# Kernel optimization log

Measured on AMD Instinct MI355X. Metric: run time of the kernel, lower is better.

## Reference

```python
import jax, jax.numpy as jnp
import numpy as np

ANCHOR_SIZES = (128.0, 256.0, 512.0)
ANCHOR_RATIOS = (0.5, 1.0, 2.0)
IOU_THR = 0.3


def _conv(x, w, b, pad):
    y = jax.lax.conv_general_dilated(
        x, w, window_strides=(1, 1), padding=[(pad, pad), (pad, pad)],
        dimension_numbers=("NCHW", "OIHW", "NCHW"))
    return y + b[None, :, None, None]


def _make_anchors(grid_h, grid_w, stride):
    # torchvision-style cell anchors (ratio-major over scales), rounded
    scales = jnp.asarray(ANCHOR_SIZES, jnp.float32)
    ratios = jnp.asarray(ANCHOR_RATIOS, jnp.float32)
    h_r = jnp.sqrt(ratios)
    w_r = 1.0 / h_r
    ws = (w_r[:, None] * scales[None, :]).reshape(-1)  # (A,)
    hs = (h_r[:, None] * scales[None, :]).reshape(-1)
    base = jnp.round(jnp.stack([-ws, -hs, ws, hs], axis=1) / 2.0)  # (A,4)
    sx = jnp.arange(grid_w, dtype=jnp.float32) * stride
    sy = jnp.arange(grid_h, dtype=jnp.float32) * stride
    yy, xx = jnp.meshgrid(sy, sx, indexing="ij")
    shifts = jnp.stack([xx, yy, xx, yy], axis=-1).reshape(-1, 4)  # (HW,4)
    return (shifts[:, None, :] + base[None, :, :]).reshape(-1, 4)  # (HW*A,4)


def _apply_box(anchors, deltas):
    w = anchors[:, 2] - anchors[:, 0]
    h = anchors[:, 3] - anchors[:, 1]
    cx = anchors[:, 0] + 0.5 * w
    cy = anchors[:, 1] + 0.5 * h
    pcx = deltas[:, 0] * w + cx
    pcy = deltas[:, 1] * h + cy
    pw = jnp.exp(deltas[:, 2]) * w
    ph = jnp.exp(deltas[:, 3]) * h
    return jnp.stack([pcx - 0.5 * pw, pcy - 0.5 * ph,
                      pcx + 0.5 * pw, pcy + 0.5 * ph], axis=1)


def _clip(boxes, img_h, img_w):
    x1 = jnp.clip(boxes[:, 0], 0.0, img_w)
    y1 = jnp.clip(boxes[:, 1], 0.0, img_h)
    x2 = jnp.clip(boxes[:, 2], 0.0, img_w)
    y2 = jnp.clip(boxes[:, 3], 0.0, img_h)
    return jnp.stack([x1, y1, x2, y2], axis=1)


def _nms_keep(boxes, scores, thr):
    # returns boolean keep mask in ORIGINAL box order (all idxs identical in
    # the source's batched_nms call, so this is plain NMS)
    n = boxes.shape[0]
    order = jnp.argsort(-scores)
    b = boxes[order]
    area = (b[:, 2] - b[:, 0]) * (b[:, 3] - b[:, 1])
    lt = jnp.maximum(b[:, None, :2], b[None, :, :2])
    rb = jnp.minimum(b[:, None, 2:], b[None, :, 2:])
    wh = jnp.clip(rb - lt, 0.0, None)
    inter = wh[..., 0] * wh[..., 1]
    iou = inter / (area[:, None] + area[None, :] - inter + 1e-9)  # (N,N)
    idx = jnp.arange(n)

    def body(i, keep):
        sup = (iou[i] > thr) & (idx > i)
        return jnp.where(keep[i], keep & ~sup, keep)

    keep_sorted = jax.lax.fori_loop(0, n, body, jnp.ones(n, bool))
    return jnp.zeros(n, bool).at[order].set(keep_sorted)


def setup_inputs() -> dict:
    key = jax.random.key(0)
    ks = jax.random.split(key, 7)
    C, H, W = 256, 32, 32
    A = len(ANCHOR_SIZES) * len(ANCHOR_RATIOS)  # 9
    return {
        "features": jax.random.normal(ks[0], (1, C, H, W), jnp.float32),
        "image_size": 512,
        "conv_w": jax.random.normal(ks[1], (512, C, 3, 3), jnp.float32) * 0.01,
        "conv_b": jnp.zeros((512,), jnp.float32),
        "cls_w": jax.random.normal(ks[2], (2 * A, 512, 1, 1), jnp.float32) * 0.01,
        "cls_b": jnp.zeros((2 * A,), jnp.float32),
        "bbox_w": jax.random.normal(ks[3], (4 * A, 512, 1, 1), jnp.float32) * 0.01,
        "bbox_b": jnp.zeros((4 * A,), jnp.float32),
    }


def reference(features, image_size, conv_w, conv_b, cls_w, cls_b, bbox_w, bbox_b):
    img_h = img_w = float(image_size)
    x = jax.nn.relu(_conv(features, conv_w, conv_b, pad=1))
    logits = _conv(x, cls_w, cls_b, pad=0)          # (1, 2A, H, W)
    bbox_pred = _conv(x, bbox_w, bbox_b, pad=0)     # (1, 4A, H, W)
    probs = jax.nn.sigmoid(logits)
    fg_scores = probs[:, 1::2, :, :].reshape(-1)    # same flatten order as torch
    grid_h, grid_w = features.shape[2], features.shape[3]
    stride = image_size // grid_h
    anchors = _make_anchors(grid_h, grid_w, float(stride))
    proposals = _apply_box(anchors, bbox_pred.reshape(-1, 4))
    proposals = _clip(proposals, img_h, img_w)
    keep = _nms_keep(proposals, fg_scores, IOU_THR)
    # fixed-shape output: suppressed boxes zeroed, plus the keep mask
    return proposals * keep[:, None].astype(proposals.dtype), probs, keep
```

## Files before the change

### kernel.cpp

```cpp
#include <hip/hip_runtime.h>
#include <math.h>

#define X_B      0
#define BBOX_B   2097152
#define PROPS_B  2244608
#define KEYS_B   2392064
#define RANK_B   2465792
#define SKEYS_B  2502656
#define SBOX_B   2576384
#define MASK_B   2725888
#define WS_NEED  13400000

typedef unsigned long long u64;
typedef double v4d __attribute__((ext_vector_type(4)));

__global__ __launch_bounds__(256, 2) void conv3x3_mfma_k(
    const float* __restrict__ feat, const float* __restrict__ w,
    const float* __restrict__ bias, float* __restrict__ xout)
{
  __shared__ float wl[9280];
  __shared__ float fl[8768];

  const int tid = threadIdx.x;
  const int bid = blockIdx.x;
  const int ct = ((bid & 7) << 2) | ((bid >> 3) >> 4);
  const int g  = (bid >> 3) & 15;
  const int co0 = ct << 4;
  const int y0  = g << 1;

  for (int i = tid; i < 8768; i += 256) fl[i] = 0.0f;

  const int lane = tid & 63, wv = tid >> 6;
  const int q = lane >> 4, n = lane & 15;
  const int wy = wv >> 1, xb = (wv & 1) << 4;
  const int xn = xb + n;

  v4d ac0 = {0.0, 0.0, 0.0, 0.0}, ac1 = {0.0, 0.0, 0.0, 0.0};
  v4d ac2 = {0.0, 0.0, 0.0, 0.0}, ac3 = {0.0, 0.0, 0.0, 0.0};
  const float4* feat4 = (const float4*)feat;

  __syncthreads();

  for (int c = 0; c < 4; ++c) {
    const int cb = c << 6;
    #pragma unroll
    for (int i = 0; i < 9; ++i) {
      const int idx4 = tid + (i << 8);
      const int co = idx4 / 144;
      const int s4 = idx4 - co * 144;
      *(float4*)&wl[co * 580 + (s4 << 2)] =
          *(const float4*)(w + (co0 + co) * 2304 + c * 576 + (s4 << 2));
    }
    #pragma unroll
    for (int i = 0; i < 8; ++i) {
      const int idx4 = tid + (i << 8);
      const int ci = idx4 >> 5;
      const int rr = (idx4 >> 3) & 3;
      const int x4 = idx4 & 7;
      const int grow = y0 - 1 + rr;
      if ((unsigned)grow < 32u) {
        const float4 v = feat4[((cb + ci) << 8) + (grow << 3) + x4];
        float* p = &fl[ci * 137 + rr * 34 + 1 + (x4 << 2)];
        p[0] = v.x; p[1] = v.y; p[2] = v.z; p[3] = v.w;
      }
    }
    __syncthreads();
    #pragma unroll
    for (int tap = 0; tap < 9; ++tap) {
      const int ky = tap / 3, kx = tap - 3 * (tap / 3);
      const float* ab = &wl[n * 580 + q * 9 + tap];
      const float* bb = &fl[q * 137 + (wy + ky) * 34 + xn + kx];
      #pragma unroll
      for (int u = 0; u < 16; u += 4) {
        ac0 = __builtin_amdgcn_mfma_f64_16x16x4f64(
            (double)ab[(u + 0) * 36], (double)bb[(u + 0) * 548], ac0, 0, 0, 0);
        ac1 = __builtin_amdgcn_mfma_f64_16x16x4f64(
            (double)ab[(u + 1) * 36], (double)bb[(u + 1) * 548], ac1, 0, 0, 0);
        ac2 = __builtin_amdgcn_mfma_f64_16x16x4f64(
            (double)ab[(u + 2) * 36], (double)bb[(u + 2) * 548], ac2, 0, 0, 0);
        ac3 = __builtin_amdgcn_mfma_f64_16x16x4f64(
            (double)ab[(u + 3) * 36], (double)bb[(u + 3) * 548], ac3, 0, 0, 0);
      }
    }
    __syncthreads();
  }

  const int pbase = (g << 6) + (wv << 4) + n;
  #pragma unroll
  for (int i = 0; i < 4; ++i) {
    const int co = co0 + q + (i << 2);
    const double s = (ac0[i] + ac1[i]) + (ac2[i] + ac3[i]);
    const double v = fmax(s + (double)bias[co], 0.0);
    xout[(co << 10) + pbase] = (float)v;
  }
}

#define CPITCH 38
#define CCHS   (18 * CPITCH)
__global__ __launch_bounds__(256) void conv3x3_relu_fb_k(
    const float* __restrict__ feat, const float* __restrict__ w,
    const float* __restrict__ bias, float* __restrict__ xout)
{
  __shared__ float il[2][8 * CCHS];
  const int cp = blockIdx.x >> 1, h = blockIdx.x & 1;
  const int tid = threadIdx.x;
  const int h16 = h << 4;
  const int co0 = cp << 1;
  for (int i = tid; i < 8 * CCHS; i += 256) { il[0][i] = 0.0f; il[1][i] = 0.0f; }
  const int yl = tid >> 4;
  const int x0 = (tid & 15) << 1;
  double aA0 = 0.0, aA1 = 0.0, aB0 = 0.0, aB1 = 0.0;
  const float4* feat4 = (const float4*)feat;
  float4 pf[5]; int pch[5], pt[5], pc4[5], pok[5];
  #pragma unroll
  for (int k = 0; k < 5; ++k) {
    const int i = tid + (k << 8);
    const int ch = i / 144, rem = i - ch * 144;
    const int t = rem >> 3, c4 = rem & 7;
    const int g = h16 - 1 + t;
    pch[k] = ch; pt[k] = t; pc4[k] = c4;
    pok[k] = (i < 1152) && ((unsigned)g < 32u);
    pf[k] = pok[k] ? feat4[(ch << 8) + (g << 3) + c4] : float4{0.f,0.f,0.f,0.f};
  }
  __syncthreads();
  for (int cc = 0; cc < 256; cc += 8) {
    const int buf = (cc >> 3) & 1;
    #pragma unroll
    for (int k = 0; k < 5; ++k)
      if (pok[k]) {
        float* p = &il[buf][pch[k] * CCHS + pt[k] * CPITCH + (pc4[k] << 2) + 1];
        p[0] = pf[k].x; p[1] = pf[k].y; p[2] = pf[k].z; p[3] = pf[k].w;
      }
    if (cc + 8 < 256) {
      #pragma unroll
      for (int k = 0; k < 5; ++k) {
        const int g = h16 - 1 + pt[k];
        if (pok[k]) pf[k] = feat4[((cc + 8 + pch[k]) << 8) + (g << 3) + pc4[k]];
      }
    }
    __syncthreads();
    #pragma unroll
    for (int cl = 0; cl < 8; ++cl) {
      const float* wAp = w + co0 * 2304 + (cc + cl) * 9;
      const float* wBp = wAp + 2304;
      double wa[9], wb[9];
      #pragma unroll
      for (int q = 0; q < 9; ++q) { wa[q] = (double)wAp[q]; wb[q] = (double)wBp[q]; }
      const float* ir = &il[buf][cl * CCHS + yl * CPITCH + x0];
      #pragma unroll
      for (int ky = 0; ky < 3; ++ky) {
        const float2 q0 = *(const float2*)(ir + ky * CPITCH);
        const float2 q1 = *(const float2*)(ir + ky * CPITCH + 2);
        const double v0 = (double)q0.x, v1 = (double)q0.y;
        const double v2 = (double)q1.x, v3 = (double)q1.y;
        aA0 += v0 * wa[3*ky+0] + v1 * wa[3*ky+1] + v2 * wa[3*ky+2];
        aA1 += v1 * wa[3*ky+0] + v2 * wa[3*ky+1] + v3 * wa[3*ky+2];
        aB0 += v0 * wb[3*ky+0] + v1 * wb[3*ky+1] + v2 * wb[3*ky+2];
        aB1 += v1 * wb[3*ky+0] + v2 * wb[3*ky+1] + v3 * wb[3*ky+2];
      }
    }
  }
  const double bA = (double)bias[co0], bB = (double)bias[co0 + 1];
  const int y = h16 + yl;
  float2 rA, rB;
  rA.x = (float)fmax(aA0 + bA, 0.0); rA.y = (float)fmax(aA1 + bA, 0.0);
  rB.x = (float)fmax(aB0 + bB, 0.0); rB.y = (float)fmax(aB1 + bB, 0.0);
  *(float2*)&xout[(co0 << 10) + (y << 5) + x0] = rA;
  *(float2*)&xout[((co0 + 1) << 10) + (y << 5) + x0] = rB;
}

__global__ __launch_bounds__(256) void head1x1_k(
    const float* __restrict__ x,
    const float* __restrict__ cls_w, const float* __restrict__ cls_b,
    const float* __restrict__ bbox_w, const float* __restrict__ bbox_b,
    float* __restrict__ out, float* __restrict__ bbox_out)
{
  __shared__ float wl[512];
  const int bid = blockIdx.x;
  const int co = bid >> 2;
  const int px = ((bid & 3) << 8) | threadIdx.x;
  const bool is_cls = co < 18;
  const float* wsrc = is_cls ? (cls_w + co * 512) : (bbox_w + (co - 18) * 512);
  for (int i = threadIdx.x; i < 512; i += 256) wl[i] = wsrc[i];
  __syncthreads();
  double acc0 = 0.0, acc1 = 0.0, acc2 = 0.0, acc3 = 0.0;
  #pragma unroll 4
  for (int c = 0; c < 512; c += 4) {
    acc0 += (double)x[((c + 0) << 10) | px] * (double)wl[c + 0];
    acc1 += (double)x[((c + 1) << 10) | px] * (double)wl[c + 1];
    acc2 += (double)x[((c + 2) << 10) | px] * (double)wl[c + 2];
    acc3 += (double)x[((c + 3) << 10) | px] * (double)wl[c + 3];
  }
  double acc = ((acc0 + acc1) + (acc2 + acc3)) +
               (double)(is_cls ? cls_b[co] : bbox_b[co - 18]);
  if (is_cls)
    out[36864 + (co << 10) + px] = (float)(1.0 / (1.0 + exp(-acc)));
  else
    bbox_out[((co - 18) << 10) + px] = (float)acc;
}

__global__ __launch_bounds__(256) void proposals_k(
    const float* __restrict__ bbox, const int* __restrict__ imgsz,
    const float* __restrict__ out, float* __restrict__ props,
    u64* __restrict__ keys, unsigned* __restrict__ rank)
{
  const int r = blockIdx.x * 256 + threadIdx.x;
  if (r >= 9216) return;
  const float4 d = ((const float4*)bbox)[r];
  const int cell = r / 9, a = r - cell * 9;
  const int ix = cell & 31, iy = cell >> 5;
  const int ri = a / 3, si = a - ri * 3;
  const double ratio = (ri == 0) ? 0.5 : (ri == 1 ? 1.0 : 2.0);
  const double scale = (si == 0) ? 128.0 : (si == 1 ? 256.0 : 512.0);
  const double hr = sqrt(ratio), wr = 1.0 / hr;
  const double bx = nearbyint(wr * scale * 0.5);
  const double by = nearbyint(hr * scale * 0.5);
  const double cx = ix * 16.0, cy = iy * 16.0;
  const double w = 2.0 * bx, hh = 2.0 * by;
  const double pcx = (double)d.x * w + cx;
  const double pcy = (double)d.y * hh + cy;
  const double pw = exp((double)d.z) * w;
  const double ph = exp((double)d.w) * hh;
  const double im = (double)imgsz[0];
  float4 o;
  o.x = (float)fmin(fmax(pcx - 0.5 * pw, 0.0), im);
  o.y = (float)fmin(fmax(pcy - 0.5 * ph, 0.0), im);
  o.z = (float)fmin(fmax(pcx + 0.5 * pw, 0.0), im);
  o.w = (float)fmin(fmax(pcy + 0.5 * ph, 0.0), im);
  ((float4*)props)[r] = o;
  const float s = out[36864 + ((2 * (r >> 10) + 1) << 10) + (r & 1023)];
  keys[r] = ((u64)__float_as_uint(s) << 32) | (unsigned)(0x7FFFFFFF - r);
  rank[r] = 0u;
}

__global__ __launch_bounds__(256) void rank_k(
    const u64* __restrict__ keys, unsigned* __restrict__ rank)
{
  const int jt = blockIdx.x % 36, ic = blockIdx.x / 36;
  const int j = jt * 256 + threadIdx.x;
  const u64 kj = keys[j];
  const int lane = threadIdx.x & 63;
  const int base = ic * 576;
  unsigned lo[9], hi[9];
  #pragma unroll
  for (int rr = 0; rr < 9; ++rr) {
    const u64 k = keys[base + rr * 64 + lane];
    lo[rr] = (unsigned)k; hi[rr] = (unsigned)(k >> 32);
  }
  unsigned cnt = 0;
  #pragma unroll
  for (int rr = 0; rr < 9; ++rr) {
    #pragma unroll
    for (int l = 0; l < 64; ++l) {
      const unsigned llo = (unsigned)__builtin_amdgcn_readlane((int)lo[rr], l);
      const unsigned lhi = (unsigned)__builtin_amdgcn_readlane((int)hi[rr], l);
      const u64 ki = ((u64)lhi << 32) | llo;
      cnt += (ki > kj) ? 1u : 0u;
    }
  }
  atomicAdd(&rank[j], cnt);
}

__global__ __launch_bounds__(256) void scatter_k(
    const u64* __restrict__ keys, const unsigned* __restrict__ rank,
    const float* __restrict__ props, u64* __restrict__ skeys,
    float4* __restrict__ sboxes)
{
  const int r = blockIdx.x * 256 + threadIdx.x;
  if (r >= 9216) return;
  const unsigned rk = rank[r];
  skeys[rk] = keys[r];
  sboxes[rk] = ((const float4*)props)[r];
}

__global__ __launch_bounds__(256) void mask_k(
    const float4* __restrict__ sb4, u64* __restrict__ mask)
{
  __shared__ __align__(16) float4 ib[64];
  const int ci = blockIdx.x;
  const int Wb = blockIdx.y << 2;
  const int i_lo = ci << 6;
  const int i_hi = min(i_lo + 64, (Wb + 4) << 6);
  if (i_lo >= i_hi) return;
  const int wv = threadIdx.x >> 6, lane = threadIdx.x & 63;
  const int W = Wb + wv;
  const int cnt = i_hi - i_lo;
  if (threadIdx.x < cnt) ib[threadIdx.x] = sb4[i_lo + threadIdx.x];
  __syncthreads();
  const float4 bj = sb4[(W << 6) + lane];
  const float areaJ = (bj.z - bj.x) * (bj.w - bj.y);
  const int n = i_hi - i_lo;
  #pragma unroll 8
  for (int k = 0; k < n; ++k) {
    const float4 bi = ib[k];
    const float areaI = (bi.z - bi.x) * (bi.w - bi.y);
    const float ix1 = fmaxf(bj.x, bi.x), iy1 = fmaxf(bj.y, bi.y);
    const float ix2 = fminf(bj.z, bi.z), iy2 = fminf(bj.w, bi.w);
    const float iw = fmaxf(ix2 - ix1, 0.0f), ih = fmaxf(iy2 - iy1, 0.0f);
    const double inter = (double)iw * (double)ih;
    const double uni = (double)areaJ + (double)areaI - inter + 1e-9;
    const bool pred = inter > 0.3 * uni;
    const u64 bal = __ballot(pred);
    const int i = i_lo + k;
    if (lane == 0) mask[(size_t)i * 144 + W] = bal;
  }
}

__global__ __launch_bounds__(1024) void sweep_out_k(
    const u64* __restrict__ mask, const u64* __restrict__ skeys,
    const float4* __restrict__ sboxes, float* __restrict__ out)
{
  extern __shared__ __align__(16) char sm[];
  u64* subm   = (u64*)sm;
  u64* supS   = subm + 9216;
  u64* keptS  = supS + 16;
  unsigned short* kpl = (unsigned short*)(keptS + 144);
  int* kcnt  = (int*)(kpl + 9216);

  const int tid = threadIdx.x;
  const int lane = tid & 63, wv = tid >> 6;
  if (tid == 0) *kcnt = 0;
  if (tid < 144) keptS[tid] = 0ULL;
  if (tid < 16) supS[tid] = 0ULL;
  if (tid < 512) {
    const int wq = tid & 7, r0 = tid >> 3;
    #pragma unroll
    for (int k = 0; k < 8; ++k) {
      const int i = r0 + (k << 6);
      subm[i * 9 + wq] = mask[(size_t)i * 144 + wq];
    }
  }
  __syncthreads();

  int Kpp = 0, Kp = 0;

  for (int sg = 0; sg < 18; ++sg) {
    const int buf = sg & 1, nb = buf ^ 1;
    const int wbase = sg << 3;
    const int ibase = wbase << 6;
    if (wv == 0) {
      u64 dacc = 0ULL;
      {
        const int wq = lane & 7;
        int j = Kpp + (lane >> 3);
        for (; j + 24 < Kp; j += 32) {
          const u64 a0 = mask[(size_t)kpl[j +  0] * 144 + wbase + wq];
          const u64 a1 = mask[(size_t)kpl[j +  8] * 144 + wbase + wq];
          const u64 a2 = mask[(size_t)kpl[j + 16] * 144 + wbase + wq];
          const u64 a3 = mask[(size_t)kpl[j + 24] * 144 + wbase + wq];
          dacc |= (a0 | a1) | (a2 | a3);
        }
        for (; j < Kp; j += 8)
          dacc |= mask[(size_t)kpl[j] * 144 + wbase + wq];
      }
      dacc |= __shfl_xor(dacc, 8, 64);
      dacc |= __shfl_xor(dacc, 16, 64);
      dacc |= __shfl_xor(dacc, 32, 64);
      u64 myAlive = (lane < 8) ? ~(supS[(buf << 3) + lane] | dacc) : 0ULL;
      if (lane < 8) supS[(buf << 3) + lane] = 0ULL;
      const u64* sub = subm + buf * 4608;
      u64 rowL8[8];
      #pragma unroll
      for (int w = 0; w < 8; ++w)
        rowL8[w] = sub[((w << 6) + lane) * 9 + w];
      int Kcur = Kp;
      #pragma unroll
      for (int w = 0; w < 8; ++w) {
        const u64 av = __shfl(myAlive, w, 64);
        if (av == 0ULL) continue;
        const u64 rowL = rowL8[w];
        u64 cand = av, keptw = 0ULL;
        while (cand) {
          const int b = (int)__builtin_ctzll(cand);
          keptw |= 1ULL << b;
          const u64 sup =
              ((u64)(unsigned)__builtin_amdgcn_readlane((int)(rowL >> 32), b)
               << 32) |
              (unsigned)__builtin_amdgcn_readlane((int)rowL, b);
          cand &= ~(sup | (1ULL << b));
        }
        if (lane == 0) keptS[wbase + w] = keptw;
        if (keptw) {
          if ((keptw >> lane) & 1ULL) {
            const int pre =
                __builtin_popcountll(keptw & ((1ULL << lane) - 1ULL));
            kpl[Kcur + pre] = (unsigned short)(ibase + (w << 6) + lane);
          }
          Kcur += __builtin_popcountll(keptw);
          u64 t = keptw;
          while (t) {
            int bs[8]; int nn = 0;
            #pragma unroll
            for (int s = 0; s < 8; ++s) {
              if (t) { bs[s] = (int)__builtin_ctzll(t); t &= t - 1ULL; nn = s + 1; }
              else bs[s] = 0;
            }
            const int kk = lane >> 3, wq = lane & 7;
            u64 r = (kk < nn) ? sub[((w << 6) + bs[kk]) * 9 + wq] : 0ULL;
            r |= __shfl_down(r, 8, 64);
            r |= __shfl_down(r, 16, 64);
            r |= __shfl_down(r, 32, 64);
            myAlive &= ~r;
          }
        }
      }
      Kpp = Kp; Kp = Kcur;
      if (lane == 0) *kcnt = Kcur;
    } else if (wv < 12) {
      if (sg + 1 < 18) {
        const int Kh = *kcnt;
        const int t6 = tid - 64;
        const int wq = t6 & 7, str = t6 >> 3;
        const int wb2 = (sg + 1) << 3;
        u64 acc = 0ULL;
        int j = str;
        for (; j + 3 * 88 < Kh; j += 4 * 88) {
          const u64 a0 = mask[(size_t)kpl[j + 0 * 88] * 144 + wb2 + wq];
          const u64 a1 = mask[(size_t)kpl[j + 1 * 88] * 144 + wb2 + wq];
          const u64 a2 = mask[(size_t)kpl[j + 2 * 88] * 144 + wb2 + wq];
          const u64 a3 = mask[(size_t)kpl[j + 3 * 88] * 144 + wb2 + wq];
          acc |= (a0 | a1) | (a2 | a3);
        }
        for (; j < Kh; j += 88)
          acc |= mask[(size_t)kpl[j] * 144 + wb2 + wq];
        if (acc) {
          atomicOr((unsigned*)&supS[(nb << 3) + wq], (unsigned)acc);
          atomicOr(((unsigned*)&supS[(nb << 3) + wq]) + 1, (unsigned)(acc >> 32));
        }
      }
    } else if (sg + 1 < 18) {
      const int s = tid - 768;
      const int wq = s & 7, r0 = s >> 3;
      const int ib2 = (sg + 1) << 9;
      const int wb2 = (sg + 1) << 3;
      #pragma unroll
      for (int k = 0; k < 16; ++k) {
        const int i = r0 + (k << 5);
        subm[nb * 4608 + i * 9 + wq] = mask[(size_t)(ib2 + i) * 144 + wb2 + wq];
      }
    }
    __syncthreads();
  }
  for (int i = tid; i < 9216; i += 1024) {
    const u64 key = skeys[i];
    const int orig = 0x7FFFFFFF - (int)(unsigned)(key & 0xFFFFFFFFULL);
    const bool kp = (keptS[i >> 6] >> (i & 63)) & 1ULL;
    float4 ob = sboxes[i];
    if (!kp) { ob.x = 0.f; ob.y = 0.f; ob.z = 0.f; ob.w = 0.f; }
    ((float4*)out)[orig] = ob;
    out[55296 + orig] = kp ? 1.0f : 0.0f;
  }
}

__global__ __launch_bounds__(1024) void nms_fallback_k(
    const float* __restrict__ props, float* __restrict__ out)
{
  __shared__ u64 wmax[16];
  __shared__ float4 curBoxS;
  const int tid = threadIdx.x, wid = tid >> 6, lane = tid & 63;
  u64 key[9];
  float4 box[9];
  #pragma unroll
  for (int j = 0; j < 9; ++j) {
    const int r = tid + (j << 10);
    box[j] = ((const float4*)props)[r];
    const float s = out[36864 + ((2 * (r >> 10) + 1) << 10) + (r & 1023)];
    key[j] = ((u64)__float_as_uint(s) << 32) | (unsigned)(0x7FFFFFFF - r);
  }
  unsigned kept = 0;
  for (;;) {
    u64 m = key[0];
    #pragma unroll
    for (int j = 1; j < 9; ++j) m = key[j] > m ? key[j] : m;
    #pragma unroll
    for (int off = 32; off; off >>= 1) {
      const u64 o = __shfl_down(m, off, 64);
      if (o > m) m = o;
    }
    if (lane == 0) wmax[wid] = m;
    __syncthreads();
    u64 K = wmax[0];
    #pragma unroll
    for (int wv2 = 1; wv2 < 16; ++wv2) { const u64 t = wmax[wv2]; if (t > K) K = t; }
    if (K == 0) break;
    #pragma unroll
    for (int j = 0; j < 9; ++j)
      if (key[j] == K) { curBoxS = box[j]; key[j] = 0; kept |= 1u << j; }
    __syncthreads();
    const float4 cb = curBoxS;
    const float areaC = (cb.z - cb.x) * (cb.w - cb.y);
    #pragma unroll
    for (int j = 0; j < 9; ++j) {
      if (key[j]) {
        const float4 b = box[j];
        const float ix1 = fmaxf(b.x, cb.x), iy1 = fmaxf(b.y, cb.y);
        const float ix2 = fminf(b.z, cb.z), iy2 = fminf(b.w, cb.w);
        const float iw = fmaxf(ix2 - ix1, 0.0f), ih = fmaxf(iy2 - iy1, 0.0f);
        const float areaB = (b.z - b.x) * (b.w - b.y);
        const double inter = (double)iw * (double)ih;
        const double uni = (double)areaB + (double)areaC - inter + 1e-9;
        if (inter > 0.3 * uni) key[j] = 0;
      }
    }
    __syncthreads();
  }
  #pragma unroll
  for (int j = 0; j < 9; ++j) {
    const int r = tid + (j << 10);
    const bool kp = (kept >> j) & 1u;
    float4 ob = box[j];
    if (!kp) { ob.x = 0.f; ob.y = 0.f; ob.z = 0.f; ob.w = 0.f; }
    ((float4*)out)[r] = ob;
    out[55296 + r] = kp ? 1.0f : 0.0f;
  }
}

extern "C" void kernel_launch(void* const* d_in, const int* in_sizes, int n_in,
                              void* d_out, int out_size, void* d_ws, size_t ws_size,
                              hipStream_t stream)
{
  const float* feat   = (const float*)d_in[0];
  const int*   imgsz  = (const int*)d_in[1];
  const float* conv_w = (const float*)d_in[2];
  const float* conv_b = (const float*)d_in[3];
  const float* cls_w  = (const float*)d_in[4];
  const float* cls_b  = (const float*)d_in[5];
  const float* bbox_w = (const float*)d_in[6];
  const float* bbox_b = (const float*)d_in[7];
  float* out = (float*)d_out;
  char*  ws  = (char*)d_ws;
  float* x      = (float*)(ws + X_B);
  float* bbox   = (float*)(ws + BBOX_B);
  float* props  = (float*)(ws + PROPS_B);
  u64*      keys  = (u64*)(ws + KEYS_B);
  unsigned* rankp = (unsigned*)(ws + RANK_B);
  u64*      skeys = (u64*)(ws + SKEYS_B);
  float4*   sboxs = (float4*)(ws + SBOX_B);
  u64*      maskp = (u64*)(ws + MASK_B);

  if (ws_size >= (size_t)WS_NEED) {
    hipLaunchKernelGGL(conv3x3_mfma_k, dim3(512), dim3(256), 0, stream,
                       feat, conv_w, conv_b, x);
    hipLaunchKernelGGL(head1x1_k, dim3(216), dim3(256), 0, stream,
                       x, cls_w, cls_b, bbox_w, bbox_b, out, bbox);
    hipLaunchKernelGGL(proposals_k, dim3(36), dim3(256), 0, stream,
                       bbox, imgsz, out, props, keys, rankp);
    hipLaunchKernelGGL(rank_k, dim3(576), dim3(256), 0, stream, keys, rankp);
    hipLaunchKernelGGL(scatter_k, dim3(36), dim3(256), 0, stream,
                       keys, rankp, props, skeys, sboxs);
    hipLaunchKernelGGL(mask_k, dim3(144, 36), dim3(256), 0, stream,
                       sboxs, maskp);
    hipLaunchKernelGGL(sweep_out_k, dim3(1), dim3(1024), 93444, stream,
                       maskp, skeys, sboxs, out);
  } else {
    hipLaunchKernelGGL(conv3x3_relu_fb_k, dim3(512), dim3(256), 0, stream,
                       feat, conv_w, conv_b, x);
    hipLaunchKernelGGL(head1x1_k, dim3(216), dim3(256), 0, stream,
                       x, cls_w, cls_b, bbox_w, bbox_b, out, bbox);
    hipLaunchKernelGGL(proposals_k, dim3(36), dim3(256), 0, stream,
                       bbox, imgsz, out, props, keys, rankp);
    hipLaunchKernelGGL(nms_fallback_k, dim3(1), dim3(1024), 0, stream,
                       props, out);
  }
}
```

Measured before the change: 249.7 us.

## Double-buffer conv3x3 MFMA LDS tiles with register-staged prefetch

Splits the input-channel loop into eight stages of 32 channels, using two LDS buffers. Global loads for the next stage go into registers and are issued before the MFMA work on the current buffer, then written to the other buffer afterwards. This hides global-memory latency behind compute and removes one barrier per stage. The cost is extra registers for the staged float4s, which may affect occupancy under the 2-blocks launch bound.

```diff
diff --git a/kernel.cpp b/kernel.cpp
--- a/kernel.cpp
+++ b/kernel.cpp
@@ -18,8 +18,8 @@
     const float* __restrict__ feat, const float* __restrict__ w,
     const float* __restrict__ bias, float* __restrict__ xout)
 {
-  __shared__ float wl[9280];
-  __shared__ float fl[8768];
+  __shared__ float wl2[2][4672];
+  __shared__ float fl2[2][4416];
 
   const int tid = threadIdx.x;
   const int bid = blockIdx.x;
@@ -28,50 +28,74 @@
   const int co0 = ct << 4;
   const int y0  = g << 1;
 
-  for (int i = tid; i < 8768; i += 256) fl[i] = 0.0f;
-
   const int lane = tid & 63, wv = tid >> 6;
   const int q = lane >> 4, n = lane & 15;
   const int wy = wv >> 1, xb = (wv & 1) << 4;
   const int xn = xb + n;
 
+  int wco[5], ws4[5]; bool wok[5];
+  #pragma unroll
+  for (int i = 0; i < 5; ++i) {
+    const int idx4 = tid + (i << 8);
+    wok[i] = idx4 < 1152;
+    const int co = idx4 / 72;
+    wco[i] = co; ws4[i] = idx4 - co * 72;
+  }
+  int fci[4], frr[4], fx4[4]; bool fok[4];
+  #pragma unroll
+  for (int i = 0; i < 4; ++i) {
+    const int idx4 = tid + (i << 8);
+    fci[i] = idx4 >> 5; frr[i] = (idx4 >> 3) & 3; fx4[i] = idx4 & 7;
+    fok[i] = ((unsigned)(y0 - 1 + frr[i]) < 32u);
+  }
+
+  for (int i = tid; i < 2 * 4416; i += 256) ((float*)fl2)[i] = 0.0f;
+
+  const float4* feat4 = (const float4*)feat;
+  float4 wr[5], fr[4];
+
+  #pragma unroll
+  for (int i = 0; i < 5; ++i)
+    if (wok[i])
+      wr[i] = *(const float4*)(w + (co0 + wco[i]) * 2304 + (ws4[i] << 2));
+  #pragma unroll
+  for (int i = 0; i < 4; ++i)
+    if (fok[i])
+      fr[i] = feat4[(fci[i] << 8) + ((y0 - 1 + frr[i]) << 3) + fx4[i]];
+  __syncthreads();
+  #pragma unroll
+  for (int i = 0; i < 5; ++i)
+    if (wok[i]) *(float4*)&wl2[0][wco[i] * 292 + (ws4[i] << 2)] = wr[i];
+  #pragma unroll
+  for (int i = 0; i < 4; ++i)
+    if (fok[i])
+      *(float4*)&fl2[0][fci[i] * 137 + frr[i] * 34 + 1 + (fx4[i] << 2)] = fr[i];
+  __syncthreads();
+
   v4d ac0 = {0.0, 0.0, 0.0, 0.0}, ac1 = {0.0, 0.0, 0.0, 0.0};
   v4d ac2 = {0.0, 0.0, 0.0, 0.0}, ac3 = {0.0, 0.0, 0.0, 0.0};
-  const float4* feat4 = (const float4*)feat;
-
-  __syncthreads();
-
-  for (int c = 0; c < 4; ++c) {
-    const int cb = c << 6;
-    #pragma unroll
-    for (int i = 0; i < 9; ++i) {
-      const int idx4 = tid + (i << 8);
-      const int co = idx4 / 144;
-      const int s4 = idx4 - co * 144;
-      *(float4*)&wl[co * 580 + (s4 << 2)] =
-          *(const float4*)(w + (co0 + co) * 2304 + c * 576 + (s4 << 2));
-    }
-    #pragma unroll
-    for (int i = 0; i < 8; ++i) {
-      const int idx4 = tid + (i << 8);
-      const int ci = idx4 >> 5;
-      const int rr = (idx4 >> 3) & 3;
-      const int x4 = idx4 & 7;
-      const int grow = y0 - 1 + rr;
-      if ((unsigned)grow < 32u) {
-        const float4 v = feat4[((cb + ci) << 8) + (grow << 3) + x4];
-        float* p = &fl[ci * 137 + rr * 34 + 1 + (x4 << 2)];
-        p[0] = v.x; p[1] = v.y; p[2] = v.z; p[3] = v.w;
-      }
-    }
-    __syncthreads();
+
+  for (int h = 0; h < 8; ++h) {
+    const int b = h & 1;
+    if (h < 7) {
+      const int cb = (h + 1) << 5;
+      #pragma unroll
+      for (int i = 0; i < 5; ++i)
+        if (wok[i])
+          wr[i] = *(const float4*)(w + (co0 + wco[i]) * 2304 +
+                                   (h + 1) * 288 + (ws4[i] << 2));
+      #pragma unroll
+      for (int i = 0; i < 4; ++i)
+        if (fok[i])
+          fr[i] = feat4[((cb + fci[i]) << 8) + ((y0 - 1 + frr[i]) << 3) + fx4[i]];
+    }
     #pragma unroll
     for (int tap = 0; tap < 9; ++tap) {
       const int ky = tap / 3, kx = tap - 3 * (tap / 3);
-      const float* ab = &wl[n * 580 + q * 9 + tap];
-      const float* bb = &fl[q * 137 + (wy + ky) * 34 + xn + kx];
-      #pragma unroll
-      for (int u = 0; u < 16; u += 4) {
+      const float* ab = &wl2[b][n * 292 + q * 9 + tap];
+      const float* bb = &fl2[b][q * 137 + (wy + ky) * 34 + xn + kx];
+      #pragma unroll
+      for (int u = 0; u < 8; u += 4) {
         ac0 = __builtin_amdgcn_mfma_f64_16x16x4f64(
             (double)ab[(u + 0) * 36], (double)bb[(u + 0) * 548], ac0, 0, 0, 0);
         ac1 = __builtin_amdgcn_mfma_f64_16x16x4f64(
@@ -81,6 +105,16 @@
         ac3 = __builtin_amdgcn_mfma_f64_16x16x4f64(
             (double)ab[(u + 3) * 36], (double)bb[(u + 3) * 548], ac3, 0, 0, 0);
       }
+    }
+    if (h < 7) {
+      const int b2 = b ^ 1;
+      #pragma unroll
+      for (int i = 0; i < 5; ++i)
+        if (wok[i]) *(float4*)&wl2[b2][wco[i] * 292 + (ws4[i] << 2)] = wr[i];
+      #pragma unroll
+      for (int i = 0; i < 4; ++i)
+        if (fok[i])
+          *(float4*)&fl2[b2][fci[i] * 137 + frr[i] * 34 + 1 + (fx4[i] << 2)] = fr[i];
     }
     __syncthreads();
   }
```

Result: slower. 266.1 us (+6.6%).
